# Kernel tuning notes

Hardware: AMD Instinct MI355X
Metric: run time of the kernel (lower is better)

Reference implementation:

```python
import jax, jax.numpy as jnp
import numpy as np

N = 100000      # nodes
E = 1600000     # edges (avg degree 16)
F_IN = 128      # in_feats
H = 128         # n_hidden
C = 40          # n_classes


def setup_inputs() -> dict:
    key = jax.random.key(0)
    ks = jax.random.split(key, 11)
    s = 0.05
    return {
        "x": jax.random.normal(ks[0], (N, F_IN), jnp.float32),
        "edge_index": jax.random.randint(ks[1], (2, E), 0, N, jnp.int32),
        # layer 1: SAGEConv(F_IN, H); lin_l has bias, lin_r has none (PyG default)
        "Wl1": jax.random.normal(ks[2], (F_IN, H), jnp.float32) * s,
        "bl1": jnp.zeros((H,), jnp.float32),
        "Wr1": jax.random.normal(ks[3], (F_IN, H), jnp.float32) * s,
        # layer 2: SAGEConv(H, H)
        "Wl2": jax.random.normal(ks[4], (H, H), jnp.float32) * s,
        "bl2": jnp.zeros((H,), jnp.float32),
        "Wr2": jax.random.normal(ks[5], (H, H), jnp.float32) * s,
        # layer 3: SAGEConv(H, C)
        "Wl3": jax.random.normal(ks[6], (H, C), jnp.float32) * s,
        "bl3": jnp.zeros((C,), jnp.float32),
        "Wr3": jax.random.normal(ks[7], (H, C), jnp.float32) * s,
    }


def _sage_conv(x, src, dst, Wl, bl, Wr):
    # PyG SAGEConv (aggr='mean', root_weight=True):
    #   out[i] = lin_l( mean_{j->i} x[j] ) + lin_r( x[i] )
    msgs = x[src]                                            # [E, d] irregular gather
    agg = jax.ops.segment_sum(msgs, dst, num_segments=N)     # [N, d]
    deg = jax.ops.segment_sum(jnp.ones((src.shape[0], 1), x.dtype), dst,
                              num_segments=N)                # [N, 1]
    agg = agg / jnp.maximum(deg, 1.0)                        # mean aggregation
    return agg @ Wl + bl + x @ Wr


def reference(x, edge_index, Wl1, bl1, Wr1, Wl2, bl2, Wr2, Wl3, bl3, Wr3):
    src, dst = edge_index[0], edge_index[1]
    h = jax.nn.relu(_sage_conv(x, src, dst, Wl1, bl1, Wr1))   # dropout is identity in eval
    h = jax.nn.relu(_sage_conv(h, src, dst, Wl2, bl2, Wr2))
    return _sage_conv(h, src, dst, Wl3, bl3, Wr3)             # [N, C]
```

## Files before the change

kernel.cpp:

```cpp
#include <hip/hip_runtime.h>

using u16 = unsigned short;
using u32 = unsigned int;
using u8 = unsigned char;
typedef __attribute__((ext_vector_type(8))) short short8;
typedef __attribute__((ext_vector_type(4))) float f32x4;

static inline int idiv_up(long a, long b) { return (int)((a + b - 1) / b); }

#define NBUCK 256
#define ECHUNK 8192
#define CAPE 9216

__device__ __forceinline__ float bflo(u32 p) { return __uint_as_float(p << 16); }
__device__ __forceinline__ float bfhi(u32 p) { return __uint_as_float(p & 0xffff0000u); }
__device__ __forceinline__ u32 f2bf1(float f) {
    u32 x = __float_as_uint(f);
    return (x + 0x7fffu + ((x >> 16) & 1u)) >> 16;
}
__device__ __forceinline__ u32 pack2(float lo, float hi) {
    return f2bf1(lo) | (f2bf1(hi) << 16);
}

__global__ __launch_bounds__(256) void k_cast(const float* __restrict__ x,
                                              u32* __restrict__ xb, long nelem) {
    long i = ((long)blockIdx.x * 256 + threadIdx.x) * 8;
    if (i >= nelem) return;
    float4 v0 = *(const float4*)(x + i);
    float4 v1 = *(const float4*)(x + i + 4);
    uint4 o;
    o.x = pack2(v0.x, v0.y);
    o.y = pack2(v0.z, v0.w);
    o.z = pack2(v1.x, v1.y);
    o.w = pack2(v1.z, v1.w);
    *(uint4*)(xb + (i >> 1)) = o;
}

__global__ __launch_bounds__(256) void k_wprep(const float* __restrict__ Wl,
                                               const float* __restrict__ Wr,
                                               u16* __restrict__ wp) {
    const int gid = blockIdx.x * 256 + threadIdx.x;
    if (gid >= 64 * 64) return;
    const int tile = gid >> 6, l = gid & 63;
    const int t = tile >> 3, s = tile & 7;
    const int n = t * 16 + (l & 15);
    const int k0 = s * 32 + (l >> 4) * 8;
    u32 w[4];
#pragma unroll
    for (int p = 0; p < 4; ++p) {
        const int ka = k0 + 2 * p, kb = ka + 1;
        const float va = (ka < 128) ? Wl[ka * 128 + n] : Wr[(ka - 128) * 128 + n];
        const float vb = (kb < 128) ? Wl[kb * 128 + n] : Wr[(kb - 128) * 128 + n];
        w[p] = pack2(va, vb);
    }
    uint4 o = {w[0], w[1], w[2], w[3]};
    *(uint4*)(wp + (size_t)gid * 8) = o;
}

__global__ __launch_bounds__(256) void k_wprep3(const float* __restrict__ Wl,
                                                const float* __restrict__ Wr,
                                                u16* __restrict__ wp) {
    const int gid = blockIdx.x * 256 + threadIdx.x;
    if (gid >= 20 * 64) return;
    const int tile = gid >> 6, l = gid & 63;
    const int t = tile >> 2, s = tile & 3;
    const int c = t * 16 + (l & 15);
    const int k0 = s * 32 + (l >> 4) * 8;
    u32 w[4];
#pragma unroll
    for (int p = 0; p < 4; ++p) {
        const int ka = k0 + 2 * p, kb = ka + 1;
        const float va = (c < 40) ? Wl[ka * 40 + c] : Wr[ka * 40 + (c - 40)];
        const float vb = (c < 40) ? Wl[kb * 40 + c] : Wr[kb * 40 + (c - 40)];
        w[p] = pack2(va, vb);
    }
    uint4 o = {w[0], w[1], w[2], w[3]};
    *(uint4*)(wp + (size_t)gid * 8) = o;
}

__global__ __launch_bounds__(256) void k_bucket(const int* __restrict__ src,
                                                const int* __restrict__ dst,
                                                int* __restrict__ cursor,
                                                u32* __restrict__ stage,
                                                int E, int rangeSize) {
    __shared__ u32 s_pay[ECHUNK];
    __shared__ u8 s_bk[ECHUNK];
    __shared__ int s_cnt[NBUCK];
    __shared__ int s_base[NBUCK];
    __shared__ int s_off[NBUCK];
    s_cnt[threadIdx.x] = 0;
    __syncthreads();
    const long e0 = (long)blockIdx.x * ECHUNK;
    const int cnt = (int)(((long)E - e0 < ECHUNK) ? (long)E - e0 : ECHUNK);
    for (int j = threadIdx.x; j < cnt; j += 256) {
        const int d = __builtin_nontemporal_load(&dst[e0 + j]);
        const int s = __builtin_nontemporal_load(&src[e0 + j]);
        const int b = d / rangeSize;
        s_pay[j] = (u32)s | ((u32)(d - b * rangeSize) << 17);
        s_bk[j] = (u8)b;
        atomicAdd(&s_cnt[b], 1);
    }
    __syncthreads();
    {
        const int c = s_cnt[threadIdx.x];
        s_base[threadIdx.x] = c ? atomicAdd(&cursor[threadIdx.x], c) : 0;
        s_off[threadIdx.x] = 0;
    }
    __syncthreads();
    for (int j = threadIdx.x; j < cnt; j += 256) {
        const int b = s_bk[j];
        const int p = atomicAdd(&s_off[b], 1);
        stage[(size_t)b * CAPE + s_base[b] + p] = s_pay[j];
    }
}

__global__ __launch_bounds__(256) void k_bscan(const int* __restrict__ cursor,
                                               int* __restrict__ bbase, int E) {
    __shared__ int wt[4];
    const int t = threadIdx.x;
    const int v = cursor[t];
    const int lane = t & 63, wid = t >> 6;
    int incl = v;
    for (int off = 1; off < 64; off <<= 1) {
        int u = __shfl_up(incl, off, 64);
        if (lane >= off) incl += u;
    }
    if (lane == 63) wt[wid] = incl;
    __syncthreads();
    int woff = 0;
    for (int w = 0; w < wid; ++w) woff += wt[w];
    bbase[t] = woff + incl - v;
    if (t == 255) bbase[256] = woff + incl;
}

__global__ __launch_bounds__(256) void k_csrlds(const u32* __restrict__ stage,
                                                const int* __restrict__ bcnt,
                                                const int* __restrict__ bbase,
                                                int* __restrict__ rowptr,
                                                float* __restrict__ invd,
                                                int* __restrict__ col,
                                                int rangeSize, int n) {
    __shared__ int s_cnt[512];
    __shared__ int s_cur[512];
    __shared__ int s_col[CAPE];
    __shared__ int wt[4];
    const int b = blockIdx.x;
    const int t = threadIdx.x;
    const int g0 = b * rangeSize;
    const size_t rd = (size_t)b * CAPE;
    const int cntb = bcnt[b];
    const int gbase = bbase[b];

    for (int i = t; i < rangeSize; i += 256) s_cnt[i] = 0;
    __syncthreads();

    for (int i = t; i < cntb; i += 256)
        atomicAdd(&s_cnt[stage[rd + i] >> 17], 1);
    __syncthreads();

    const int i0 = 2 * t, i1 = 2 * t + 1;
    const int c0 = (i0 < rangeSize) ? s_cnt[i0] : 0;
    const int c1 = (i1 < rangeSize) ? s_cnt[i1] : 0;
    const int sum = c0 + c1;
    const int lane = t & 63, wid = t >> 6;
    int incl = sum;
    for (int off = 1; off < 64; off <<= 1) {
        int u = __shfl_up(incl, off, 64);
        if (lane >= off) incl += u;
    }
    if (lane == 63) wt[wid] = incl;
    __syncthreads();
    int woff = 0;
    for (int w = 0; w < wid; ++w) woff += wt[w];
    const int excl = woff + incl - sum;
    if (i0 < rangeSize) {
        s_cur[i0] = excl;
        const int g = g0 + i0;
        if (g <= n) rowptr[g] = gbase + excl;
        if (g < n) invd[g] = 1.0f / fmaxf((float)c0, 1.0f);
    }
    if (i1 < rangeSize) {
        s_cur[i1] = excl + c0;
        const int g = g0 + i1;
        if (g <= n) rowptr[g] = gbase + excl + c0;
        if (g < n) invd[g] = 1.0f / fmaxf((float)c1, 1.0f);
    }
    __syncthreads();

    for (int i = t; i < cntb; i += 256) {
        const u32 v = stage[rd + i];
        const int p = atomicAdd(&s_cur[v >> 17], 1);
        s_col[p] = (int)(v & 0x1FFFFu);
    }
    __syncthreads();

    for (int i = t; i < cntb; i += 256) col[gbase + i] = s_col[i];
}

#define ACC8(A, B, V)                                                          \
    A.x += bflo(V.x); A.y += bfhi(V.x); A.z += bflo(V.y); A.w += bfhi(V.y);    \
    B.x += bflo(V.z); B.y += bfhi(V.z); B.z += bflo(V.w); B.w += bfhi(V.w);

__global__ __launch_bounds__(256, 8) void k_aggmm(const u16* __restrict__ xb,
                                                  const int* __restrict__ rowptr,
                                                  const int* __restrict__ col,
                                                  const float* __restrict__ invd,
                                                  const u16* __restrict__ wp,
                                                  const float* __restrict__ bl,
                                                  u16* __restrict__ outb, int n) {
    __shared__ __align__(16) u16 s_a[64][136];
    const int row0 = blockIdx.x * 64;
    const int tid = threadIdx.x;
    const int l = tid & 15;

#pragma unroll
    for (int it = 0; it < 4; ++it) {
        const int r = it * 16 + (tid >> 4);
        const int node = row0 + r;
        float4 eA0 = {0.f, 0.f, 0.f, 0.f}, eA1 = {0.f, 0.f, 0.f, 0.f};
        float4 eB0 = {0.f, 0.f, 0.f, 0.f}, eB1 = {0.f, 0.f, 0.f, 0.f};
        float inv = 0.f;
        if (node < n) {
            inv = invd[node];
            const int s0 = rowptr[node], s1 = rowptr[node + 1];
            for (int cb = s0; cb < s1; cb += 16) {
                const int cnt = min(16, s1 - cb);
                const int cc = (cb + l < s1) ? col[cb + l] : 0;
                int j = 0;
                for (; j + 4 <= cnt; j += 4) {
                    const int n0 = __shfl(cc, j, 16);
                    const int n1 = __shfl(cc, j + 1, 16);
                    const int n2 = __shfl(cc, j + 2, 16);
                    const int n3 = __shfl(cc, j + 3, 16);
                    const uint4 v0 = *(const uint4*)(xb + (size_t)n0 * 128 + 8 * l);
                    const uint4 v1 = *(const uint4*)(xb + (size_t)n1 * 128 + 8 * l);
                    const uint4 v2 = *(const uint4*)(xb + (size_t)n2 * 128 + 8 * l);
                    const uint4 v3 = *(const uint4*)(xb + (size_t)n3 * 128 + 8 * l);
                    ACC8(eA0, eA1, v0); ACC8(eB0, eB1, v1);
                    ACC8(eA0, eA1, v2); ACC8(eB0, eB1, v3);
                }
                for (; j < cnt; ++j) {
                    const int nn = __shfl(cc, j, 16);
                    const uint4 v = *(const uint4*)(xb + (size_t)nn * 128 + 8 * l);
                    ACC8(eA0, eA1, v);
                }
            }
        }
        uint4 o;
        o.x = pack2((eA0.x + eB0.x) * inv, (eA0.y + eB0.y) * inv);
        o.y = pack2((eA0.z + eB0.z) * inv, (eA0.w + eB0.w) * inv);
        o.z = pack2((eA1.x + eB1.x) * inv, (eA1.y + eB1.y) * inv);
        o.w = pack2((eA1.z + eB1.z) * inv, (eA1.w + eB1.w) * inv);
        *(uint4*)(&s_a[r][8 * l]) = o;
    }
    __syncthreads();

    const int l64 = tid & 63;
    const int w = tid >> 6;
    const int rloc = w * 16 + (l64 & 15);
    const int q = l64 >> 4;
    const int rowc = min(row0 + rloc, n - 1);

    f32x4 acc[8];
#pragma unroll
    for (int t = 0; t < 8; ++t) acc[t] = (f32x4){0.f, 0.f, 0.f, 0.f};

#pragma unroll
    for (int s = 0; s < 8; ++s) {
        const short8 a = (s < 4)
            ? *(const short8*)(&s_a[rloc][s * 32 + q * 8])
            : *(const short8*)(xb + (size_t)rowc * 128 + (s - 4) * 32 + q * 8);
#pragma unroll
        for (int t = 0; t < 8; ++t) {
            const short8 b = *(const short8*)(wp + ((size_t)(t * 8 + s) * 64 + l64) * 8);
            acc[t] = __builtin_amdgcn_mfma_f32_16x16x32_bf16(a, b, acc[t], 0, 0, 0);
        }
    }

    const int rowb = row0 + w * 16 + q * 4;
#pragma unroll
    for (int t = 0; t < 8; ++t) {
        const float bias = bl[t * 16 + (l64 & 15)];
#pragma unroll
        for (int r = 0; r < 4; ++r) {
            const int row = rowb + r;
            if (row < n) {
                const float o = fmaxf(acc[t][r] + bias, 0.f);
                outb[(size_t)row * 128 + t * 16 + (l64 & 15)] = (u16)f2bf1(o);
            }
        }
    }
}

__global__ __launch_bounds__(256, 4) void k_mm40f(const u16* __restrict__ hb,
                                                  const u16* __restrict__ wp,
                                                  const float* __restrict__ bl,
                                                  u16* __restrict__ t40b,
                                                  float* __restrict__ r40, int n) {
    __shared__ __align__(16) u16 s_a[64][136];
    const int row0 = blockIdx.x * 64;
    const int tid = threadIdx.x;

#pragma unroll
    for (int it = 0; it < 4; ++it) {
        const int idx = tid + it * 256;
        const int r = idx >> 4, c8 = idx & 15;
        const int row = row0 + r;
        uint4 v = {0u, 0u, 0u, 0u};
        if (row < n) v = *(const uint4*)(hb + (size_t)row * 128 + c8 * 8);
        *(uint4*)(&s_a[r][c8 * 8]) = v;
    }
    __syncthreads();

    const int l = tid & 63;
    const int w = tid >> 6;
    const int rloc = w * 16 + (l & 15);
    const int q = l >> 4;

    short8 afr[4];
#pragma unroll
    for (int s = 0; s < 4; ++s)
        afr[s] = *(const short8*)(&s_a[rloc][s * 32 + q * 8]);

    f32x4 acc[5];
#pragma unroll
    for (int t = 0; t < 5; ++t) acc[t] = (f32x4){0.f, 0.f, 0.f, 0.f};

#pragma unroll
    for (int t = 0; t < 5; ++t) {
#pragma unroll
        for (int s = 0; s < 4; ++s) {
            const short8 b = *(const short8*)(wp + ((size_t)(t * 4 + s) * 64 + l) * 8);
            acc[t] = __builtin_amdgcn_mfma_f32_16x16x32_bf16(afr[s], b, acc[t], 0, 0, 0);
        }
    }

    const int rowb = row0 + w * 16 + q * 4;
#pragma unroll
    for (int t = 0; t < 5; ++t) {
        const int c = t * 16 + (l & 15);
        const float bias = (c >= 40) ? bl[c - 40] : 0.f;
#pragma unroll
        for (int r = 0; r < 4; ++r) {
            const int row = rowb + r;
            if (row < n) {
                if (c < 40)
                    t40b[(size_t)row * 40 + c] = (u16)f2bf1(acc[t][r]);
                else
                    r40[(size_t)row * 40 + (c - 40)] = acc[t][r] + bias;
            }
        }
    }
}

#define ACC4(A, V)                                                     \
    A.x += bflo(V.x); A.y += bfhi(V.x); A.z += bflo(V.y); A.w += bfhi(V.y);

__global__ __launch_bounds__(256) void k_agg40(const u16* __restrict__ t40b,
                                               const float* __restrict__ r40,
                                               const int* __restrict__ rowptr,
                                               const int* __restrict__ col,
                                               const float* __restrict__ invd,
                                               float* __restrict__ out, int n) {
    const int tt = blockIdx.x * 256 + threadIdx.x;
    const int node = tt >> 4;
    if (node >= n) return;
    const int l = tt & 15;
    const bool act = l < 10;
    const int s0 = rowptr[node], s1 = rowptr[node + 1];
    float4 a0 = {0.f, 0.f, 0.f, 0.f};
    float4 a1 = {0.f, 0.f, 0.f, 0.f};
    for (int cb = s0; cb < s1; cb += 16) {
        const int cnt = min(16, s1 - cb);
        const int cc = (cb + l < s1) ? col[cb + l] : 0;
        int j = 0;
        for (; j + 4 <= cnt; j += 4) {
            const int n0 = __shfl(cc, j, 16);
            const int n1 = __shfl(cc, j + 1, 16);
            const int n2 = __shfl(cc, j + 2, 16);
            const int n3 = __shfl(cc, j + 3, 16);
            if (act) {
                const uint2 v0 = *(const uint2*)(t40b + (size_t)n0 * 40 + 4 * l);
                const uint2 v1 = *(const uint2*)(t40b + (size_t)n1 * 40 + 4 * l);
                const uint2 v2 = *(const uint2*)(t40b + (size_t)n2 * 40 + 4 * l);
                const uint2 v3 = *(const uint2*)(t40b + (size_t)n3 * 40 + 4 * l);
                ACC4(a0, v0); ACC4(a1, v1); ACC4(a0, v2); ACC4(a1, v3);
            }
        }
        for (; j < cnt; ++j) {
            const int nn = __shfl(cc, j, 16);
            if (act) {
                const uint2 v = *(const uint2*)(t40b + (size_t)nn * 40 + 4 * l);
                ACC4(a0, v);
            }
        }
    }
    if (act) {
        const float inv = invd[node];
        const float4 rv = *(const float4*)(r40 + (size_t)node * 40 + 4 * l);
        float4 o;
        o.x = fmaf(a0.x + a1.x, inv, rv.x);
        o.y = fmaf(a0.y + a1.y, inv, rv.y);
        o.z = fmaf(a0.z + a1.z, inv, rv.z);
        o.w = fmaf(a0.w + a1.w, inv, rv.w);
        *(float4*)(out + (size_t)node * 40 + 4 * l) = o;
    }
}

extern "C" void kernel_launch(void* const* d_in, const int* in_sizes, int n_in,
                              void* d_out, int out_size, void* d_ws, size_t ws_size,
                              hipStream_t stream) {
    const float* x   = (const float*)d_in[0];
    const int*   ei  = (const int*)d_in[1];
    const float* Wl1 = (const float*)d_in[2];
    const float* bl1 = (const float*)d_in[3];
    const float* Wr1 = (const float*)d_in[4];
    const float* Wl2 = (const float*)d_in[5];
    const float* bl2 = (const float*)d_in[6];
    const float* Wr2 = (const float*)d_in[7];
    const float* Wl3 = (const float*)d_in[8];
    const float* bl3 = (const float*)d_in[9];
    const float* Wr3 = (const float*)d_in[10];
    float* out = (float*)d_out;

    const int N = in_sizes[0] / 128;
    const int E = in_sizes[1] / 2;
    const int* src = ei;
    const int* dst = ei + E;

    auto align1k = [](size_t v) { return (v + 1023) & ~(size_t)1023; };
    const size_t NB16 = (size_t)N * 128 * sizeof(u16);

    char* ws = (char*)d_ws;
    size_t off = 0;
    float* invd     = (float*)(ws + off); off += align1k((size_t)N * 4);
    int*   rowptr   = (int*)(ws + off);   off += align1k((size_t)(N + 1) * 4);
    int*   cursor   = (int*)(ws + off);   off += align1k(NBUCK * 4);
    int*   bbase    = (int*)(ws + off);   off += align1k((NBUCK + 1) * 4);
    u16*   wp1      = (u16*)(ws + off);   off += align1k(64 * 1024);
    u16*   wp2      = (u16*)(ws + off);   off += align1k(64 * 1024);
    u16*   wp3      = (u16*)(ws + off);   off += align1k(20 * 1024);
    int*   col      = (int*)(ws + off);   off += align1k((size_t)E * 4);
    u32*   stage    = (u32*)(ws + off);   off += align1k((size_t)NBUCK * CAPE * 4);
    u16*   xb       = (u16*)(ws + off);   off += align1k(NB16);
    char*  regionY  = (ws + off);         off += align1k(NB16);
    u16*   h1b  = (u16*)regionY;
    u16*   h2b  = xb;
    u16*   t40b = (u16*)regionY;
    float* r40  = (float*)(regionY + align1k((size_t)N * 40 * sizeof(u16)));

    const int nPB        = idiv_up(E, ECHUNK);
    const int castBlocks = idiv_up((long)N * 128, 2048);
    const int agg40Blk   = idiv_up((long)N * 16, 256);
    const int mmBlocks   = idiv_up(N, 64);
    const int rangeSize  = idiv_up(N, NBUCK);

    k_cast<<<castBlocks, 256, 0, stream>>>(x, (u32*)xb, (long)N * 128);
    k_wprep<<<16, 256, 0, stream>>>(Wl1, Wr1, wp1);
    k_wprep<<<16, 256, 0, stream>>>(Wl2, Wr2, wp2);
    k_wprep3<<<5, 256, 0, stream>>>(Wl3, Wr3, wp3);

    hipMemsetAsync(cursor, 0, NBUCK * sizeof(int), stream);
    k_bucket<<<nPB, 256, 0, stream>>>(src, dst, cursor, stage, E, rangeSize);
    k_bscan<<<1, 256, 0, stream>>>(cursor, bbase, E);
    k_csrlds<<<NBUCK, 256, 0, stream>>>(stage, cursor, bbase, rowptr, invd, col,
                                        rangeSize, N);

    k_aggmm<<<mmBlocks, 256, 0, stream>>>(xb, rowptr, col, invd, wp1, bl1, h1b, N);

    k_aggmm<<<mmBlocks, 256, 0, stream>>>(h1b, rowptr, col, invd, wp2, bl2, h2b, N);

    k_mm40f<<<mmBlocks, 256, 0, stream>>>(h2b, wp3, bl3, t40b, r40, N);
    k_agg40<<<agg40Blk, 256, 0, stream>>>(t40b, r40, rowptr, col, invd, out, N);
}
```

Baseline: 294.9 us.

## Merge weight-prep kernels, fold bucket scan into CSR build, widen aggregation lanes

The three weight-packing kernels become one launch, and the bucket prefix scan is recomputed inside each CSR-build block, so a separate scan kernel is no longer needed. Both cut launch overhead. In the layer aggregation, each node now gets 32 lanes loading 8-byte slices, with up to 8 neighbor loads in flight, instead of 16 lanes loading 16-byte slices. The matmul output is staged through shared memory so global stores are coalesced 16-byte writes. The trade-off is redundant scan work in every block, narrower per-lane loads, and an extra barrier.

```diff
diff --git a/kernel.cpp b/kernel.cpp
--- a/kernel.cpp
+++ b/kernel.cpp
@@ -36,46 +36,53 @@
     *(uint4*)(xb + (i >> 1)) = o;
 }
 
-__global__ __launch_bounds__(256) void k_wprep(const float* __restrict__ Wl,
-                                               const float* __restrict__ Wr,
-                                               u16* __restrict__ wp) {
-    const int gid = blockIdx.x * 256 + threadIdx.x;
-    if (gid >= 64 * 64) return;
-    const int tile = gid >> 6, l = gid & 63;
-    const int t = tile >> 3, s = tile & 7;
-    const int n = t * 16 + (l & 15);
-    const int k0 = s * 32 + (l >> 4) * 8;
-    u32 w[4];
-#pragma unroll
-    for (int p = 0; p < 4; ++p) {
-        const int ka = k0 + 2 * p, kb = ka + 1;
-        const float va = (ka < 128) ? Wl[ka * 128 + n] : Wr[(ka - 128) * 128 + n];
-        const float vb = (kb < 128) ? Wl[kb * 128 + n] : Wr[(kb - 128) * 128 + n];
-        w[p] = pack2(va, vb);
-    }
-    uint4 o = {w[0], w[1], w[2], w[3]};
-    *(uint4*)(wp + (size_t)gid * 8) = o;
-}
-
-__global__ __launch_bounds__(256) void k_wprep3(const float* __restrict__ Wl,
-                                                const float* __restrict__ Wr,
-                                                u16* __restrict__ wp) {
-    const int gid = blockIdx.x * 256 + threadIdx.x;
-    if (gid >= 20 * 64) return;
-    const int tile = gid >> 6, l = gid & 63;
-    const int t = tile >> 2, s = tile & 3;
-    const int c = t * 16 + (l & 15);
-    const int k0 = s * 32 + (l >> 4) * 8;
-    u32 w[4];
-#pragma unroll
-    for (int p = 0; p < 4; ++p) {
-        const int ka = k0 + 2 * p, kb = ka + 1;
-        const float va = (c < 40) ? Wl[ka * 40 + c] : Wr[ka * 40 + (c - 40)];
-        const float vb = (c < 40) ? Wl[kb * 40 + c] : Wr[kb * 40 + (c - 40)];
-        w[p] = pack2(va, vb);
-    }
-    uint4 o = {w[0], w[1], w[2], w[3]};
-    *(uint4*)(wp + (size_t)gid * 8) = o;
+__global__ __launch_bounds__(256) void k_wprepall(const float* __restrict__ Wl1,
+                                                  const float* __restrict__ Wr1,
+                                                  const float* __restrict__ Wl2,
+                                                  const float* __restrict__ Wr2,
+                                                  const float* __restrict__ Wl3,
+                                                  const float* __restrict__ Wr3,
+                                                  u16* __restrict__ wp1,
+                                                  u16* __restrict__ wp2,
+                                                  u16* __restrict__ wp3) {
+    const int b = blockIdx.x;
+    if (b < 32) {
+        const float* Wl = (b < 16) ? Wl1 : Wl2;
+        const float* Wr = (b < 16) ? Wr1 : Wr2;
+        u16* wp = (b < 16) ? wp1 : wp2;
+        const int gid = (b & 15) * 256 + threadIdx.x;
+        const int tile = gid >> 6, l = gid & 63;
+        const int t = tile >> 3, s = tile & 7;
+        const int n = t * 16 + (l & 15);
+        const int k0 = s * 32 + (l >> 4) * 8;
+        u32 w[4];
+#pragma unroll
+        for (int p = 0; p < 4; ++p) {
+            const int ka = k0 + 2 * p, kb = ka + 1;
+            const float va = (ka < 128) ? Wl[ka * 128 + n] : Wr[(ka - 128) * 128 + n];
+            const float vb = (kb < 128) ? Wl[kb * 128 + n] : Wr[(kb - 128) * 128 + n];
+            w[p] = pack2(va, vb);
+        }
+        uint4 o = {w[0], w[1], w[2], w[3]};
+        *(uint4*)(wp + (size_t)gid * 8) = o;
+    } else {
+        const int gid = (b - 32) * 256 + threadIdx.x;
+        if (gid >= 20 * 64) return;
+        const int tile = gid >> 6, l = gid & 63;
+        const int t = tile >> 2, s = tile & 3;
+        const int c = t * 16 + (l & 15);
+        const int k0 = s * 32 + (l >> 4) * 8;
+        u32 w[4];
+#pragma unroll
+        for (int p = 0; p < 4; ++p) {
+            const int ka = k0 + 2 * p, kb = ka + 1;
+            const float va = (c < 40) ? Wl3[ka * 40 + c] : Wr3[ka * 40 + (c - 40)];
+            const float vb = (c < 40) ? Wl3[kb * 40 + c] : Wr3[kb * 40 + (c - 40)];
+            w[p] = pack2(va, vb);
+        }
+        uint4 o = {w[0], w[1], w[2], w[3]};
+        *(uint4*)(wp3 + (size_t)gid * 8) = o;
+    }
 }
 
 __global__ __launch_bounds__(256) void k_bucket(const int* __restrict__ src,
@@ -114,28 +121,8 @@
     }
 }
 
-__global__ __launch_bounds__(256) void k_bscan(const int* __restrict__ cursor,
-                                               int* __restrict__ bbase, int E) {
-    __shared__ int wt[4];
-    const int t = threadIdx.x;
-    const int v = cursor[t];
-    const int lane = t & 63, wid = t >> 6;
-    int incl = v;
-    for (int off = 1; off < 64; off <<= 1) {
-        int u = __shfl_up(incl, off, 64);
-        if (lane >= off) incl += u;
-    }
-    if (lane == 63) wt[wid] = incl;
-    __syncthreads();
-    int woff = 0;
-    for (int w = 0; w < wid; ++w) woff += wt[w];
-    bbase[t] = woff + incl - v;
-    if (t == 255) bbase[256] = woff + incl;
-}
-
 __global__ __launch_bounds__(256) void k_csrlds(const u32* __restrict__ stage,
-                                                const int* __restrict__ bcnt,
-                                                const int* __restrict__ bbase,
+                                                const int* __restrict__ cursor,
                                                 int* __restrict__ rowptr,
                                                 float* __restrict__ invd,
                                                 int* __restrict__ col,
@@ -144,12 +131,29 @@
     __shared__ int s_cur[512];
     __shared__ int s_col[CAPE];
     __shared__ int wt[4];
+    __shared__ int sh_gbase;
     const int b = blockIdx.x;
     const int t = threadIdx.x;
     const int g0 = b * rangeSize;
     const size_t rd = (size_t)b * CAPE;
-    const int cntb = bcnt[b];
-    const int gbase = bbase[b];
+
+    {
+        const int v = cursor[t];
+        const int lane = t & 63, wid = t >> 6;
+        int incl = v;
+        for (int off = 1; off < 64; off <<= 1) {
+            int u = __shfl_up(incl, off, 64);
+            if (lane >= off) incl += u;
+        }
+        if (lane == 63) wt[wid] = incl;
+        __syncthreads();
+        int woff = 0;
+        for (int w = 0; w < wid; ++w) woff += wt[w];
+        if (t == b) sh_gbase = woff + incl - v;
+    }
+    __syncthreads();
+    const int cntb = cursor[b];
+    const int gbase = sh_gbase;
 
     for (int i = t; i < rangeSize; i += 256) s_cnt[i] = 0;
     __syncthreads();
@@ -168,6 +172,7 @@
         int u = __shfl_up(incl, off, 64);
         if (lane >= off) incl += u;
     }
+    __syncthreads();
     if (lane == 63) wt[wid] = incl;
     __syncthreads();
     int woff = 0;
@@ -197,9 +202,8 @@
     for (int i = t; i < cntb; i += 256) col[gbase + i] = s_col[i];
 }
 
-#define ACC8(A, B, V)                                                          \
-    A.x += bflo(V.x); A.y += bfhi(V.x); A.z += bflo(V.y); A.w += bfhi(V.y);    \
-    B.x += bflo(V.z); B.y += bfhi(V.z); B.z += bflo(V.w); B.w += bfhi(V.w);
+#define ACC4(A, V)                                                     \
+    A.x += bflo(V.x); A.y += bfhi(V.x); A.z += bflo(V.y); A.w += bfhi(V.y);
 
 __global__ __launch_bounds__(256, 8) void k_aggmm(const u16* __restrict__ xb,
                                                   const int* __restrict__ rowptr,
@@ -211,47 +215,64 @@
     __shared__ __align__(16) u16 s_a[64][136];
     const int row0 = blockIdx.x * 64;
     const int tid = threadIdx.x;
-    const int l = tid & 15;
-
-#pragma unroll
-    for (int it = 0; it < 4; ++it) {
-        const int r = it * 16 + (tid >> 4);
+
+    const int l32 = tid & 31;
+#pragma unroll
+    for (int it = 0; it < 8; ++it) {
+        const int r = it * 8 + (tid >> 5);
         const int node = row0 + r;
-        float4 eA0 = {0.f, 0.f, 0.f, 0.f}, eA1 = {0.f, 0.f, 0.f, 0.f};
-        float4 eB0 = {0.f, 0.f, 0.f, 0.f}, eB1 = {0.f, 0.f, 0.f, 0.f};
+        float4 a0 = {0.f, 0.f, 0.f, 0.f};
+        float4 a1 = {0.f, 0.f, 0.f, 0.f};
         float inv = 0.f;
         if (node < n) {
             inv = invd[node];
             const int s0 = rowptr[node], s1 = rowptr[node + 1];
-            for (int cb = s0; cb < s1; cb += 16) {
-                const int cnt = min(16, s1 - cb);
-                const int cc = (cb + l < s1) ? col[cb + l] : 0;
+            for (int cb = s0; cb < s1; cb += 32) {
+                const int cnt = min(32, s1 - cb);
+                const int cc = (cb + l32 < s1) ? col[cb + l32] : 0;
                 int j = 0;
+                for (; j + 8 <= cnt; j += 8) {
+                    const int n0 = __shfl(cc, j, 32);
+                    const int n1 = __shfl(cc, j + 1, 32);
+                    const int n2 = __shfl(cc, j + 2, 32);
+                    const int n3 = __shfl(cc, j + 3, 32);
+                    const int n4 = __shfl(cc, j + 4, 32);
+                    const int n5 = __shfl(cc, j + 5, 32);
+                    const int n6 = __shfl(cc, j + 6, 32);
+                    const int n7 = __shfl(cc, j + 7, 32);
+                    const uint2 v0 = *(const uint2*)(xb + (size_t)n0 * 128 + 4 * l32);
+                    const uint2 v1 = *(const uint2*)(xb + (size_t)n1 * 128 + 4 * l32);
+                    const uint2 v2 = *(const uint2*)(xb + (size_t)n2 * 128 + 4 * l32);
+                    const uint2 v3 = *(const uint2*)(xb + (size_t)n3 * 128 + 4 * l32);
+                    const uint2 v4 = *(const uint2*)(xb + (size_t)n4 * 128 + 4 * l32);
+                    const uint2 v5 = *(const uint2*)(xb + (size_t)n5 * 128 + 4 * l32);
+                    const uint2 v6 = *(const uint2*)(xb + (size_t)n6 * 128 + 4 * l32);
+                    const uint2 v7 = *(const uint2*)(xb + (size_t)n7 * 128 + 4 * l32);
+                    ACC4(a0, v0); ACC4(a1, v1); ACC4(a0, v2); ACC4(a1, v3);
+                    ACC4(a0, v4); ACC4(a1, v5); ACC4(a0, v6); ACC4(a1, v7);
+                }
                 for (; j + 4 <= cnt; j += 4) {
-                    const int n0 = __shfl(cc, j, 16);
-                    const int n1 = __shfl(cc, j + 1, 16);
-                    const int n2 = __shfl(cc, j + 2, 16);
-                    const int n3 = __shfl(cc, j + 3, 16);
-                    const uint4 v0 = *(const uint4*)(xb + (size_t)n0 * 128 + 8 * l);
-                    const uint4 v1 = *(const uint4*)(xb + (size_t)n1 * 128 + 8 * l);
-                    const uint4 v2 = *(const uint4*)(xb + (size_t)n2 * 128 + 8 * l);
-                    const uint4 v3 = *(const uint4*)(xb + (size_t)n3 * 128 + 8 * l);
-                    ACC8(eA0, eA1, v0); ACC8(eB0, eB1, v1);
-                    ACC8(eA0, eA1, v2); ACC8(eB0, eB1, v3);
+                    const int n0 = __shfl(cc, j, 32);
+                    const int n1 = __shfl(cc, j + 1, 32);
+                    const int n2 = __shfl(cc, j + 2, 32);
+                    const int n3 = __shfl(cc, j + 3, 32);
+                    const uint2 v0 = *(const uint2*)(xb + (size_t)n0 * 128 + 4 * l32);
+                    const uint2 v1 = *(const uint2*)(xb + (size_t)n1 * 128 + 4 * l32);
+                    const uint2 v2 = *(const uint2*)(xb + (size_t)n2 * 128 + 4 * l32);
+                    const uint2 v3 = *(const uint2*)(xb + (size_t)n3 * 128 + 4 * l32);
+                    ACC4(a0, v0); ACC4(a1, v1); ACC4(a0, v2); ACC4(a1, v3);
                 }
                 for (; j < cnt; ++j) {
-                    const int nn = __shfl(cc, j, 16);
-                    const uint4 v = *(const uint4*)(xb + (size_t)nn * 128 + 8 * l);
-                    ACC8(eA0, eA1, v);
+                    const int nn = __shfl(cc, j, 32);
+                    const uint2 v = *(const uint2*)(xb + (size_t)nn * 128 + 4 * l32);
+                    ACC4(a0, v);
                 }
             }
         }
-        uint4 o;
-        o.x = pack2((eA0.x + eB0.x) * inv, (eA0.y + eB0.y) * inv);
-        o.y = pack2((eA0.z + eB0.z) * inv, (eA0.w + eB0.w) * inv);
-        o.z = pack2((eA1.x + eB1.x) * inv, (eA1.y + eB1.y) * inv);
-        o.w = pack2((eA1.z + eB1.z) * inv, (eA1.w + eB1.w) * inv);
-        *(uint4*)(&s_a[r][8 * l]) = o;
+        uint2 o;
+        o.x = pack2((a0.x + a1.x) * inv, (a0.y + a1.y) * inv);
+        o.y = pack2((a0.z + a1.z) * inv, (a0.w + a1.w) * inv);
+        *(uint2*)(&s_a[r][4 * l32]) = o;
     }
     __syncthreads();
 
@@ -277,18 +298,25 @@
         }
     }
 
-    const int rowb = row0 + w * 16 + q * 4;
+    const int cb16 = l64 & 15;
+    const int rowl = w * 16 + q * 4;
 #pragma unroll
     for (int t = 0; t < 8; ++t) {
-        const float bias = bl[t * 16 + (l64 & 15)];
+        const float bias = bl[t * 16 + cb16];
 #pragma unroll
         for (int r = 0; r < 4; ++r) {
-            const int row = rowb + r;
-            if (row < n) {
-                const float o = fmaxf(acc[t][r] + bias, 0.f);
-                outb[(size_t)row * 128 + t * 16 + (l64 & 15)] = (u16)f2bf1(o);
-            }
-        }
+            const float o = fmaxf(acc[t][r] + bias, 0.f);
+            s_a[rowl + r][t * 16 + cb16] = (u16)f2bf1(o);
+        }
+    }
+    __syncthreads();
+#pragma unroll
+    for (int it = 0; it < 4; ++it) {
+        const int idx = tid + it * 256;
+        const int r = idx >> 4, c8 = idx & 15;
+        const int row = row0 + r;
+        if (row < n)
+            *(uint4*)(outb + (size_t)row * 128 + c8 * 8) = *(const uint4*)(&s_a[r][c8 * 8]);
     }
 }
 
@@ -352,9 +380,6 @@
         }
     }
 }
-
-#define ACC4(A, V)                                                     \
-    A.x += bflo(V.x); A.y += bfhi(V.x); A.z += bflo(V.y); A.w += bfhi(V.y);
 
 __global__ __launch_bounds__(256) void k_agg40(const u16* __restrict__ t40b,
                                                const float* __restrict__ r40,
@@ -436,7 +461,6 @@
     float* invd     = (float*)(ws + off); off += align1k((size_t)N * 4);
     int*   rowptr   = (int*)(ws + off);   off += align1k((size_t)(N + 1) * 4);
     int*   cursor   = (int*)(ws + off);   off += align1k(NBUCK * 4);
-    int*   bbase    = (int*)(ws + off);   off += align1k((NBUCK + 1) * 4);
     u16*   wp1      = (u16*)(ws + off);   off += align1k(64 * 1024);
     u16*   wp2      = (u16*)(ws + off);   off += align1k(64 * 1024);
     u16*   wp3      = (u16*)(ws + off);   off += align1k(20 * 1024);
@@ -456,14 +480,11 @@
     const int rangeSize  = idiv_up(N, NBUCK);
 
     k_cast<<<castBlocks, 256, 0, stream>>>(x, (u32*)xb, (long)N * 128);
-    k_wprep<<<16, 256, 0, stream>>>(Wl1, Wr1, wp1);
-    k_wprep<<<16, 256, 0, stream>>>(Wl2, Wr2, wp2);
-    k_wprep3<<<5, 256, 0, stream>>>(Wl3, Wr3, wp3);
+    k_wprepall<<<37, 256, 0, stream>>>(Wl1, Wr1, Wl2, Wr2, Wl3, Wr3, wp1, wp2, wp3);
 
     hipMemsetAsync(cursor, 0, NBUCK * sizeof(int), stream);
     k_bucket<<<nPB, 256, 0, stream>>>(src, dst, cursor, stage, E, rangeSize);
-    k_bscan<<<1, 256, 0, stream>>>(cursor, bbase, E);
-    k_csrlds<<<NBUCK, 256, 0, stream>>>(stage, cursor, bbase, rowptr, invd, col,
+    k_csrlds<<<NBUCK, 256, 0, stream>>>(stage, cursor, rowptr, invd, col,
                                         rangeSize, N);
 
     k_aggmm<<<mmBlocks, 256, 0, stream>>>(xb, rowptr, col, invd, wp1, bl1, h1b, N);
```

Result: faster. 287.7 us (-2.4%).
